# Kernel tuning notes

Measured on AMD Instinct MI355X. Metric: run time of the kernel, lower is better.

Reference implementation:

```python
import jax, jax.numpy as jnp
import numpy as np

B, H, S, D, KG = 1, 8, 1024, 64, 10

def setup_inputs() -> dict:
    key = jax.random.key(0)
    ks = jax.random.split(key, 16)
    n = jax.random.normal
    u = jax.random.uniform
    return {
        'Q': n(ks[0], (B, H, S, D), dtype=jnp.float32),
        'K': n(ks[1], (B, H, S, D), dtype=jnp.float32),
        'V': n(ks[2], (B, H, S, D), dtype=jnp.float32),
        'distance_matrix': u(ks[3], (B, H, S, S), dtype=jnp.float32) * 10.0,
        'energy_matrix': u(ks[4], (B, H, S, S), dtype=jnp.float32) * 5.0,
        'mask': jnp.ones((B, H, S, S), dtype=jnp.int32),
        'mu_D': n(ks[5], (KG,), dtype=jnp.float32),
        'sigma_D': u(ks[6], (KG,), dtype=jnp.float32) + 0.5,  # keep sigma positive
        'b_D': n(ks[7], (KG,), dtype=jnp.float32) * 0.1,
        'mu_E': n(ks[8], (KG,), dtype=jnp.float32),
        'sigma_E': u(ks[9], (KG,), dtype=jnp.float32) + 0.5,
        'b_E': n(ks[10], (KG,), dtype=jnp.float32) * 0.1,
        'W1': n(ks[11], (KG, KG), dtype=jnp.float32) / np.sqrt(KG),
        'b1': jnp.zeros((KG,), dtype=jnp.float32),
        'W2': n(ks[12], (1, KG), dtype=jnp.float32) / np.sqrt(KG),
        'b2': jnp.zeros((1,), dtype=jnp.float32),
    }


def _rbf_mlp_bias(x, b, mu, sigma, W1, b1, W2, b2):
    # x: [B,H,S,S] -> Gaussian RBF features over K kernels, then small MLP -> [B,H,S,S]
    z = (x[..., None] + b - mu) / sigma                      # [B,H,S,S,K]
    inv_norm = 1.0 / (jnp.sqrt(2.0 * jnp.pi) * sigma)
    psi = jnp.exp(-0.5 * z * z) * inv_norm                   # [B,H,S,S,K]
    h = jax.nn.gelu(jnp.einsum('bhijk,lk->bhijl', psi, W1) + b1, approximate=False)
    return (jnp.einsum('bhijk,lk->bhijl', h, W2) + b2)[..., 0]


def reference(Q, K, V, distance_matrix, energy_matrix, mask,
              mu_D, sigma_D, b_D, mu_E, sigma_E, b_E, W1, b1, W2, b2):
    d_model = Q.shape[-1]
    scores = jnp.einsum('bhid,bhjd->bhij', Q, K) / np.sqrt(d_model * 2)
    scores = scores + _rbf_mlp_bias(distance_matrix, b_D, mu_D, sigma_D, W1, b1, W2, b2)
    scores = scores + _rbf_mlp_bias(energy_matrix, b_E, mu_E, sigma_E, W1, b1, W2, b2)
    scores = jnp.where(mask == 0, jnp.float32(-1e9), scores)
    attn = jax.nn.softmax(scores, axis=-1)
    return jnp.einsum('bhij,bhjd->bhid', attn, V)
```

## Files before the change

### kernel.cpp

```cpp
#include <hip/hip_runtime.h>
#include <math.h>

#define Hn 8
#define Sn 1024
#define Dn 64
#define KG 10

#define TN 2048
#define RD 10.25f
#define RE 5.125f

#define KS 4

typedef __attribute__((ext_vector_type(8))) short bf16x8;
typedef __attribute__((ext_vector_type(4))) float f32x4;
typedef unsigned short u16;
typedef unsigned int u32;

__device__ inline float bf2f(u16 u) {
    union { u32 i; float f; } v;
    v.i = ((u32)u) << 16;
    return v.f;
}

__device__ inline u16 f2bf(float f) {
    union { float f; u32 i; } v;
    v.f = f;
    u32 i = v.i;
    return (u16)((i + 0x7FFFu + ((i >> 16) & 1u)) >> 16);
}

__device__ float bias_eval(float x,
                           const float* __restrict__ mu, const float* __restrict__ sg,
                           const float* __restrict__ bb,
                           const float* __restrict__ W1, const float* __restrict__ b1,
                           const float* __restrict__ W2, const float* __restrict__ b2) {
    const float inv_s2pi = 0.39894228040143267794f;
    float psi[KG];
#pragma unroll
    for (int k = 0; k < KG; k++) {
        float s = sg[k];
        float z = (x + bb[k] - mu[k]) / s;
        psi[k] = __expf(-0.5f * z * z) * (inv_s2pi / s);
    }
    float out = b2[0];
#pragma unroll
    for (int l = 0; l < KG; l++) {
        float a = b1[l];
#pragma unroll
        for (int k = 0; k < KG; k++) a += psi[k] * W1[l * KG + k];
        float g = 0.5f * a * (1.0f + erff(a * 0.70710678118654752440f));
        out += g * W2[l];
    }
    return out;
}

#define QK4 262144
#define VTN 524288

__global__ __launch_bounds__(256) void prep_kernel(
    const float* __restrict__ Q, const float* __restrict__ K, const float* __restrict__ V,
    const float* __restrict__ muD, const float* __restrict__ sgD, const float* __restrict__ bD,
    const float* __restrict__ muE, const float* __restrict__ sgE, const float* __restrict__ bE,
    const float* __restrict__ W1, const float* __restrict__ b1,
    const float* __restrict__ W2, const float* __restrict__ b2,
    u32* __restrict__ tab, u16* __restrict__ Qb, u16* __restrict__ Kb, u16* __restrict__ VTi)
{
    int id = blockIdx.x * 256 + threadIdx.x;
    if (id < 2 * TN) {
        int which = (id >= TN);
        int idx = id & (TN - 1);
        float h = (which ? RE : RD) / (float)TN;
        float x0 = idx * h;
        float v0, v1;
        if (which) {
            v0 = bias_eval(x0,     muE, sgE, bE, W1, b1, W2, b2);
            v1 = bias_eval(x0 + h, muE, sgE, bE, W1, b1, W2, b2);
        } else {
            v0 = bias_eval(x0,     muD, sgD, bD, W1, b1, W2, b2);
            v1 = bias_eval(x0 + h, muD, sgD, bD, W1, b1, W2, b2);
        }
        tab[id] = (u32)f2bf(v0) | ((u32)f2bf(v1 - v0) << 16);
    } else if (id < 2 * TN + QK4) {
        int i = id - 2 * TN;
        int arr = i >> 17;
        i &= (1 << 17) - 1;
        float4 v = ((const float4*)(arr ? K : Q))[i];
        ushort4 o;
        o.x = f2bf(v.x); o.y = f2bf(v.y); o.z = f2bf(v.z); o.w = f2bf(v.w);
        ((ushort4*)(arr ? Kb : Qb))[i] = o;
    } else if (id < 2 * TN + QK4 + VTN) {
        int g = id - (2 * TN + QK4);
        int h = g >> 16;
        int d = (g >> 10) & 63;
        int s = g & 1023;
        int t = s >> 5, q = (s >> 3) & 3, j = s & 7;
        int src_s = (t << 5) + (q << 2) + (j & 3) + ((j >> 2) << 4);
        VTi[g] = f2bf(V[(((size_t)h << 10) + src_s) * Dn + d]);
    }
}

__device__ inline float lerp_tab(const u32* __restrict__ st, float x, float invh) {
    float tf = x * invh;
    int i = (int)tf;
    i = max(0, min(i, TN - 1));
    float fr = tf - (float)i;
    u32 p = st[i];
    return fmaf(bf2f((u16)(p >> 16)), fr, bf2f((u16)p));
}

__global__ __launch_bounds__(256, 4) void attn_kernel(
    const u16* __restrict__ Qb, const u16* __restrict__ Kb, const u16* __restrict__ VTi,
    const float* __restrict__ Dm, const float* __restrict__ Em, const int* __restrict__ Mk,
    const u32* __restrict__ gtab,
    float* __restrict__ Up, float* __restrict__ Mp, float* __restrict__ Lp)
{
    __shared__ __align__(16) u32 sTab[2 * TN];
    __shared__ float sO[4][16][68];
    __shared__ float sM[4][16], sL[4][16];

    const int tid = threadIdx.x;
    {
        const uint4* g4 = (const uint4*)gtab;
        uint4* s4 = (uint4*)sTab;
#pragma unroll
        for (int i = 0; i < 4; i++) s4[tid + 256 * i] = g4[tid + 256 * i];
    }
    __syncthreads();

    const int h    = blockIdx.y;
    const int qb   = blockIdx.x;
    const int ks   = blockIdx.z;
    const int q0   = qb * 16;
    const int wave = tid >> 6;
    const int lane = tid & 63;
    const int quad = lane >> 4;
    const int l16  = lane & 15;

    const u16* Qh = Qb  + (size_t)h * Sn * Dn;
    const u16* Kh = Kb  + (size_t)h * Sn * Dn;
    const u16* Vh = VTi + (size_t)h * Dn * Sn;
    const float* Dh = Dm + (size_t)h * Sn * Sn + (size_t)(q0 + l16) * Sn;
    const float* Eh = Em + (size_t)h * Sn * Sn + (size_t)(q0 + l16) * Sn;
    const int*   Mh = Mk + (size_t)h * Sn * Sn + (size_t)(q0 + l16) * Sn;
    const float invhD = (float)TN / RD;
    const float invhE = (float)TN / RE;
    const float scale = 0.08838834764831845f;

    const bf16x8 bQ0 = *(const bf16x8*)(Qh + (q0 + l16) * Dn + quad * 8);
    const bf16x8 bQ1 = *(const bf16x8*)(Qh + (q0 + l16) * Dn + 32 + quad * 8);

    f32x4 O0 = {0.f, 0.f, 0.f, 0.f}, O1 = O0, O2 = O0, O3 = O0;
    float m_run = -1e30f, l_run = 0.f;

    for (int t = 0; t < 2; t++) {
        const int k0 = ks * 256 + wave * 64 + t * 32;

        const float4 Dv0 = *(const float4*)(Dh + k0 + quad * 4);
        const float4 Dv1 = *(const float4*)(Dh + k0 + 16 + quad * 4);
        const float4 Ev0 = *(const float4*)(Eh + k0 + quad * 4);
        const float4 Ev1 = *(const float4*)(Eh + k0 + 16 + quad * 4);
        const int4   Mv0 = *(const int4*)(Mh + k0 + quad * 4);
        const int4   Mv1 = *(const int4*)(Mh + k0 + 16 + quad * 4);

        const u16* kr = Kh + (size_t)(k0 + l16) * Dn + quad * 8;
        const bf16x8 aK00 = *(const bf16x8*)(kr);
        const bf16x8 aK01 = *(const bf16x8*)(kr + 32);
        const bf16x8 aK10 = *(const bf16x8*)(kr + 16 * Dn);
        const bf16x8 aK11 = *(const bf16x8*)(kr + 16 * Dn + 32);

        const u16* vr = Vh + k0 + quad * 8;
        const bf16x8 bV0 = *(const bf16x8*)(vr + (size_t)(l16)      * Sn);
        const bf16x8 bV1 = *(const bf16x8*)(vr + (size_t)(16 + l16) * Sn);
        const bf16x8 bV2 = *(const bf16x8*)(vr + (size_t)(32 + l16) * Sn);
        const bf16x8 bV3 = *(const bf16x8*)(vr + (size_t)(48 + l16) * Sn);

        __builtin_amdgcn_sched_barrier(0);

        f32x4 s0 = {0.f, 0.f, 0.f, 0.f}, s1 = s0;
        s0 = __builtin_amdgcn_mfma_f32_16x16x32_bf16(aK00, bQ0, s0, 0, 0, 0);
        s0 = __builtin_amdgcn_mfma_f32_16x16x32_bf16(aK01, bQ1, s0, 0, 0, 0);
        s1 = __builtin_amdgcn_mfma_f32_16x16x32_bf16(aK10, bQ0, s1, 0, 0, 0);
        s1 = __builtin_amdgcn_mfma_f32_16x16x32_bf16(aK11, bQ1, s1, 0, 0, 0);

        const float dv0[4] = {Dv0.x, Dv0.y, Dv0.z, Dv0.w};
        const float dv1[4] = {Dv1.x, Dv1.y, Dv1.z, Dv1.w};
        const float ev0[4] = {Ev0.x, Ev0.y, Ev0.z, Ev0.w};
        const float ev1[4] = {Ev1.x, Ev1.y, Ev1.z, Ev1.w};
        const int   mv0[4] = {Mv0.x, Mv0.y, Mv0.z, Mv0.w};
        const int   mv1[4] = {Mv1.x, Mv1.y, Mv1.z, Mv1.w};

        float sc0[4], sc1[4];
#pragma unroll
        for (int r = 0; r < 4; r++) {
            float v0 = s0[r] * scale + lerp_tab(sTab, dv0[r], invhD)
                                     + lerp_tab(sTab + TN, ev0[r], invhE);
            v0 = fminf(fmaxf(v0, -80.f), 80.f);
            sc0[r] = (mv0[r] == 0) ? -1e9f : v0;
            float v1 = s1[r] * scale + lerp_tab(sTab, dv1[r], invhD)
                                     + lerp_tab(sTab + TN, ev1[r], invhE);
            v1 = fminf(fmaxf(v1, -80.f), 80.f);
            sc1[r] = (mv1[r] == 0) ? -1e9f : v1;
        }

        float mloc = fmaxf(fmaxf(fmaxf(sc0[0], sc0[1]), fmaxf(sc0[2], sc0[3])),
                           fmaxf(fmaxf(sc1[0], sc1[1]), fmaxf(sc1[2], sc1[3])));
        mloc = fmaxf(mloc, __shfl_xor(mloc, 16, 64));
        mloc = fmaxf(mloc, __shfl_xor(mloc, 32, 64));

        const float mn = fmaxf(m_run, mloc);
        const float al = __expf(m_run - mn);
        m_run = mn;

        float p0[4], p1[4], ll = 0.f;
#pragma unroll
        for (int r = 0; r < 4; r++) {
            p0[r] = __expf(sc0[r] - mn);
            p1[r] = __expf(sc1[r] - mn);
            ll += p0[r] + p1[r];
        }
        ll += __shfl_xor(ll, 16, 64);
        ll += __shfl_xor(ll, 32, 64);
        l_run = l_run * al + ll;

        bf16x8 aP;
#pragma unroll
        for (int r = 0; r < 4; r++) {
            aP[r]     = (short)f2bf(p0[r]);
            aP[4 + r] = (short)f2bf(p1[r]);
        }

        const float a0 = __shfl(al, quad * 4 + 0, 64);
        const float a1 = __shfl(al, quad * 4 + 1, 64);
        const float a2 = __shfl(al, quad * 4 + 2, 64);
        const float a3 = __shfl(al, quad * 4 + 3, 64);
        O0[0] *= a0; O0[1] *= a1; O0[2] *= a2; O0[3] *= a3;
        O1[0] *= a0; O1[1] *= a1; O1[2] *= a2; O1[3] *= a3;
        O2[0] *= a0; O2[1] *= a1; O2[2] *= a2; O2[3] *= a3;
        O3[0] *= a0; O3[1] *= a1; O3[2] *= a2; O3[3] *= a3;

        O0 = __builtin_amdgcn_mfma_f32_16x16x32_bf16(aP, bV0, O0, 0, 0, 0);
        O1 = __builtin_amdgcn_mfma_f32_16x16x32_bf16(aP, bV1, O1, 0, 0, 0);
        O2 = __builtin_amdgcn_mfma_f32_16x16x32_bf16(aP, bV2, O2, 0, 0, 0);
        O3 = __builtin_amdgcn_mfma_f32_16x16x32_bf16(aP, bV3, O3, 0, 0, 0);
    }

    if (lane < 16) {
        sM[wave][lane] = m_run;
        sL[wave][lane] = l_run;
    }
#pragma unroll
    for (int r = 0; r < 4; r++) {
        sO[wave][quad * 4 + r][ 0 + l16] = O0[r];
        sO[wave][quad * 4 + r][16 + l16] = O1[r];
        sO[wave][quad * 4 + r][32 + l16] = O2[r];
        sO[wave][quad * 4 + r][48 + l16] = O3[r];
    }
    __syncthreads();

    const int row = tid >> 4;
    const int c4  = (tid & 15) * 4;
    float mg = sM[0][row];
#pragma unroll
    for (int w = 1; w < 4; w++) mg = fmaxf(mg, sM[w][row]);
    float fac[4], lg = 0.f;
#pragma unroll
    for (int w = 0; w < 4; w++) {
        fac[w] = __expf(sM[w][row] - mg);
        lg += sL[w][row] * fac[w];
    }

    float acc[4];
#pragma unroll
    for (int c = 0; c < 4; c++) {
        acc[c] = 0.f;
#pragma unroll
        for (int w = 0; w < 4; w++) acc[c] += sO[w][row][c4 + c] * fac[w];
    }

    const int pbase = ((h * 64 + qb) * KS + ks) * 16 + row;
    float4 ov = {acc[0], acc[1], acc[2], acc[3]};
    *(float4*)(Up + (size_t)pbase * 64 + c4) = ov;
    if ((tid & 15) == 0) {
        Mp[pbase] = mg;
        Lp[pbase] = lg;
    }
}

__global__ __launch_bounds__(256) void combine_kernel(
    const float* __restrict__ Up, const float* __restrict__ Mp,
    const float* __restrict__ Lp, float* __restrict__ out)
{
    const int g  = blockIdx.x * 256 + threadIdx.x;
    const int r  = g >> 4;
    const int c4 = (g & 15) * 4;
    const int h  = r >> 10;
    const int s  = r & 1023;
    const int qb = s >> 4;
    const int r16 = s & 15;
    const int base = ((h * 64 + qb) * KS) * 16 + r16;

    float m[KS], l[KS];
#pragma unroll
    for (int k = 0; k < KS; k++) {
        m[k] = Mp[base + k * 16];
        l[k] = Lp[base + k * 16];
    }
    float M = m[0];
#pragma unroll
    for (int k = 1; k < KS; k++) M = fmaxf(M, m[k]);
    float f[KS], L = 0.f;
#pragma unroll
    for (int k = 0; k < KS; k++) {
        f[k] = __expf(m[k] - M);
        L += l[k] * f[k];
    }
    const float inv = 1.0f / L;

    float acc[4] = {0.f, 0.f, 0.f, 0.f};
#pragma unroll
    for (int k = 0; k < KS; k++) {
        const float4 u = *(const float4*)(Up + (size_t)(base + k * 16) * 64 + c4);
        acc[0] += u.x * f[k]; acc[1] += u.y * f[k];
        acc[2] += u.z * f[k]; acc[3] += u.w * f[k];
    }
    float4 ov = {acc[0] * inv, acc[1] * inv, acc[2] * inv, acc[3] * inv};
    *(float4*)(out + (size_t)r * Dn + c4) = ov;
}

extern "C" void kernel_launch(void* const* d_in, const int* in_sizes, int n_in,
                              void* d_out, int out_size, void* d_ws, size_t ws_size,
                              hipStream_t stream) {
    const float* Q    = (const float*)d_in[0];
    const float* K    = (const float*)d_in[1];
    const float* V    = (const float*)d_in[2];
    const float* Dm   = (const float*)d_in[3];
    const float* Em   = (const float*)d_in[4];
    const int*   Mask = (const int*)d_in[5];
    const float* muD  = (const float*)d_in[6];
    const float* sgD  = (const float*)d_in[7];
    const float* bD   = (const float*)d_in[8];
    const float* muE  = (const float*)d_in[9];
    const float* sgE  = (const float*)d_in[10];
    const float* bE   = (const float*)d_in[11];
    const float* W1   = (const float*)d_in[12];
    const float* b1   = (const float*)d_in[13];
    const float* W2   = (const float*)d_in[14];
    const float* b2   = (const float*)d_in[15];

    u32* tab = (u32*)d_ws;
    u16* Qb  = (u16*)((char*)d_ws + 2 * TN * 4);
    u16* Kb  = Qb + (size_t)Hn * Sn * Dn;
    u16* VTi = Kb + (size_t)Hn * Sn * Dn;
    float* Up = (float*)(VTi + (size_t)Hn * Sn * Dn);
    float* Mp = Up + (size_t)Hn * 64 * KS * 16 * 64;
    float* Lp = Mp + (size_t)Hn * 64 * KS * 16;

    const int prep_threads = 2 * TN + QK4 + VTN;
    prep_kernel<<<prep_threads / 256, 256, 0, stream>>>(
        Q, K, V, muD, sgD, bD, muE, sgE, bE, W1, b1, W2, b2,
        tab, Qb, Kb, VTi);

    dim3 grid(Sn / 16, Hn, KS);
    attn_kernel<<<grid, 256, 0, stream>>>(Qb, Kb, VTi, Dm, Em, Mask, tab,
                                          Up, Mp, Lp);

    combine_kernel<<<(Hn * Sn * 16) / 256, 256, 0, stream>>>(Up, Mp, Lp,
                                                             (float*)d_out);
}
```

Baseline: 182.1 us.

## Write per-wave partials directly to global and merge all in combine kernel

```diff
diff --git a/kernel.cpp b/kernel.cpp
--- a/kernel.cpp
+++ b/kernel.cpp
@@ -11,6 +11,7 @@
 #define RE 5.125f
 
 #define KS 4
+#define NP (KS * 4)
 
 typedef __attribute__((ext_vector_type(8))) short bf16x8;
 typedef __attribute__((ext_vector_type(4))) float f32x4;
@@ -109,15 +110,13 @@
     return fmaf(bf2f((u16)(p >> 16)), fr, bf2f((u16)p));
 }
 
-__global__ __launch_bounds__(256, 4) void attn_kernel(
+__global__ __launch_bounds__(256, 8) void attn_kernel(
     const u16* __restrict__ Qb, const u16* __restrict__ Kb, const u16* __restrict__ VTi,
     const float* __restrict__ Dm, const float* __restrict__ Em, const int* __restrict__ Mk,
     const u32* __restrict__ gtab,
     float* __restrict__ Up, float* __restrict__ Mp, float* __restrict__ Lp)
 {
     __shared__ __align__(16) u32 sTab[2 * TN];
-    __shared__ float sO[4][16][68];
-    __shared__ float sM[4][16], sL[4][16];
 
     const int tid = threadIdx.x;
     {
@@ -174,8 +173,6 @@
         const bf16x8 bV1 = *(const bf16x8*)(vr + (size_t)(16 + l16) * Sn);
         const bf16x8 bV2 = *(const bf16x8*)(vr + (size_t)(32 + l16) * Sn);
         const bf16x8 bV3 = *(const bf16x8*)(vr + (size_t)(48 + l16) * Sn);
-
-        __builtin_amdgcn_sched_barrier(0);
 
         f32x4 s0 = {0.f, 0.f, 0.f, 0.f}, s1 = s0;
         s0 = __builtin_amdgcn_mfma_f32_16x16x32_bf16(aK00, bQ0, s0, 0, 0, 0);
@@ -245,45 +242,20 @@
         O3 = __builtin_amdgcn_mfma_f32_16x16x32_bf16(aP, bV3, O3, 0, 0, 0);
     }
 
+    const int p = ks * 4 + wave;
+    const size_t pg = (size_t)(h * 64 + qb) * NP + p;
+    float* up = Up + pg * 16 * 64;
+#pragma unroll
+    for (int r = 0; r < 4; r++) {
+        const int row = quad * 4 + r;
+        up[row * 64 +  0 + l16] = O0[r];
+        up[row * 64 + 16 + l16] = O1[r];
+        up[row * 64 + 32 + l16] = O2[r];
+        up[row * 64 + 48 + l16] = O3[r];
+    }
     if (lane < 16) {
-        sM[wave][lane] = m_run;
-        sL[wave][lane] = l_run;
-    }
-#pragma unroll
-    for (int r = 0; r < 4; r++) {
-        sO[wave][quad * 4 + r][ 0 + l16] = O0[r];
-        sO[wave][quad * 4 + r][16 + l16] = O1[r];
-        sO[wave][quad * 4 + r][32 + l16] = O2[r];
-        sO[wave][quad * 4 + r][48 + l16] = O3[r];
-    }
-    __syncthreads();
-
-    const int row = tid >> 4;
-    const int c4  = (tid & 15) * 4;
-    float mg = sM[0][row];
-#pragma unroll
-    for (int w = 1; w < 4; w++) mg = fmaxf(mg, sM[w][row]);
-    float fac[4], lg = 0.f;
-#pragma unroll
-    for (int w = 0; w < 4; w++) {
-        fac[w] = __expf(sM[w][row] - mg);
-        lg += sL[w][row] * fac[w];
-    }
-
-    float acc[4];
-#pragma unroll
-    for (int c = 0; c < 4; c++) {
-        acc[c] = 0.f;
-#pragma unroll
-        for (int w = 0; w < 4; w++) acc[c] += sO[w][row][c4 + c] * fac[w];
-    }
-
-    const int pbase = ((h * 64 + qb) * KS + ks) * 16 + row;
-    float4 ov = {acc[0], acc[1], acc[2], acc[3]};
-    *(float4*)(Up + (size_t)pbase * 64 + c4) = ov;
-    if ((tid & 15) == 0) {
-        Mp[pbase] = mg;
-        Lp[pbase] = lg;
+        Mp[pg * 16 + lane] = m_run;
+        Lp[pg * 16 + lane] = l_run;
     }
 }
 
@@ -298,20 +270,20 @@
     const int s  = r & 1023;
     const int qb = s >> 4;
     const int r16 = s & 15;
-    const int base = ((h * 64 + qb) * KS) * 16 + r16;
-
-    float m[KS], l[KS];
-#pragma unroll
-    for (int k = 0; k < KS; k++) {
-        m[k] = Mp[base + k * 16];
-        l[k] = Lp[base + k * 16];
+    const size_t pg0 = (size_t)(h * 64 + qb) * NP;
+
+    float m[NP], l[NP];
+#pragma unroll
+    for (int k = 0; k < NP; k++) {
+        m[k] = Mp[(pg0 + k) * 16 + r16];
+        l[k] = Lp[(pg0 + k) * 16 + r16];
     }
     float M = m[0];
 #pragma unroll
-    for (int k = 1; k < KS; k++) M = fmaxf(M, m[k]);
-    float f[KS], L = 0.f;
-#pragma unroll
-    for (int k = 0; k < KS; k++) {
+    for (int k = 1; k < NP; k++) M = fmaxf(M, m[k]);
+    float f[NP], L = 0.f;
+#pragma unroll
+    for (int k = 0; k < NP; k++) {
         f[k] = __expf(m[k] - M);
         L += l[k] * f[k];
     }
@@ -319,8 +291,8 @@
 
     float acc[4] = {0.f, 0.f, 0.f, 0.f};
 #pragma unroll
-    for (int k = 0; k < KS; k++) {
-        const float4 u = *(const float4*)(Up + (size_t)(base + k * 16) * 64 + c4);
+    for (int k = 0; k < NP; k++) {
+        const float4 u = *(const float4*)(Up + ((pg0 + k) * 16 + r16) * 64 + c4);
         acc[0] += u.x * f[k]; acc[1] += u.y * f[k];
         acc[2] += u.z * f[k]; acc[3] += u.w * f[k];
     }
@@ -353,8 +325,8 @@
     u16* Kb  = Qb + (size_t)Hn * Sn * Dn;
     u16* VTi = Kb + (size_t)Hn * Sn * Dn;
     float* Up = (float*)(VTi + (size_t)Hn * Sn * Dn);
-    float* Mp = Up + (size_t)Hn * 64 * KS * 16 * 64;
-    float* Lp = Mp + (size_t)Hn * 64 * KS * 16;
+    float* Mp = Up + (size_t)Hn * 64 * NP * 16 * 64;
+    float* Lp = Mp + (size_t)Hn * 64 * NP * 16;
 
     const int prep_threads = 2 * TN + QK4 + VTN;
     prep_kernel<<<prep_threads / 256, 256, 0, stream>>>(
```

Result: slower. 191.0 us (+4.9%).

## Split bias evaluation into separate streaming kernel producing fp16 bias tensor

Applied to the files above, without the earlier changes.

```diff
diff --git a/kernel.cpp b/kernel.cpp
--- a/kernel.cpp
+++ b/kernel.cpp
@@ -14,6 +14,9 @@
 
 typedef __attribute__((ext_vector_type(8))) short bf16x8;
 typedef __attribute__((ext_vector_type(4))) float f32x4;
+typedef _Float16 f16;
+typedef __attribute__((ext_vector_type(4))) _Float16 f16x4;
+typedef __attribute__((ext_vector_type(8))) _Float16 f16x8;
 typedef unsigned short u16;
 typedef unsigned int u32;
 
@@ -109,16 +112,13 @@
     return fmaf(bf2f((u16)(p >> 16)), fr, bf2f((u16)p));
 }
 
-__global__ __launch_bounds__(256, 4) void attn_kernel(
-    const u16* __restrict__ Qb, const u16* __restrict__ Kb, const u16* __restrict__ VTi,
+#define CB_GROUPS (Hn * Sn * Sn / 8)
+
+__global__ __launch_bounds__(256) void bias_kernel(
     const float* __restrict__ Dm, const float* __restrict__ Em, const int* __restrict__ Mk,
-    const u32* __restrict__ gtab,
-    float* __restrict__ Up, float* __restrict__ Mp, float* __restrict__ Lp)
+    const u32* __restrict__ gtab, f16* __restrict__ Cb)
 {
     __shared__ __align__(16) u32 sTab[2 * TN];
-    __shared__ float sO[4][16][68];
-    __shared__ float sM[4][16], sL[4][16];
-
     const int tid = threadIdx.x;
     {
         const uint4* g4 = (const uint4*)gtab;
@@ -127,7 +127,42 @@
         for (int i = 0; i < 4; i++) s4[tid + 256 * i] = g4[tid + 256 * i];
     }
     __syncthreads();
-
+    const float invhD = (float)TN / RD;
+    const float invhE = (float)TN / RE;
+
+    for (int g = blockIdx.x * 256 + tid; g < CB_GROUPS; g += gridDim.x * 256) {
+        const size_t base = (size_t)g * 8;
+
+        const float4 d0 = *(const float4*)(Dm + base);
+        const float4 d1 = *(const float4*)(Dm + base + 4);
+        const float4 e0 = *(const float4*)(Em + base);
+        const float4 e1 = *(const float4*)(Em + base + 4);
+        const int4   m0 = *(const int4*)(Mk + base);
+        const int4   m1 = *(const int4*)(Mk + base + 4);
+
+        const float dv[8] = {d0.x, d0.y, d0.z, d0.w, d1.x, d1.y, d1.z, d1.w};
+        const float ev[8] = {e0.x, e0.y, e0.z, e0.w, e1.x, e1.y, e1.z, e1.w};
+        const int   mv[8] = {m0.x, m0.y, m0.z, m0.w, m1.x, m1.y, m1.z, m1.w};
+
+        f16x8 o;
+#pragma unroll
+        for (int j = 0; j < 8; j++) {
+            float b = lerp_tab(sTab, dv[j], invhD) + lerp_tab(sTab + TN, ev[j], invhE);
+            o[j] = (f16)((mv[j] == 0) ? -60000.0f : b);
+        }
+        ((f16x8*)Cb)[g] = o;
+    }
+}
+
+__global__ __launch_bounds__(256, 6) void attn_kernel(
+    const u16* __restrict__ Qb, const u16* __restrict__ Kb, const u16* __restrict__ VTi,
+    const f16* __restrict__ Cb,
+    float* __restrict__ Up, float* __restrict__ Mp, float* __restrict__ Lp)
+{
+    __shared__ float sO[4][16][68];
+    __shared__ float sM[4][16], sL[4][16];
+
+    const int tid  = threadIdx.x;
     const int h    = blockIdx.y;
     const int qb   = blockIdx.x;
     const int ks   = blockIdx.z;
@@ -140,11 +175,7 @@
     const u16* Qh = Qb  + (size_t)h * Sn * Dn;
     const u16* Kh = Kb  + (size_t)h * Sn * Dn;
     const u16* Vh = VTi + (size_t)h * Dn * Sn;
-    const float* Dh = Dm + (size_t)h * Sn * Sn + (size_t)(q0 + l16) * Sn;
-    const float* Eh = Em + (size_t)h * Sn * Sn + (size_t)(q0 + l16) * Sn;
-    const int*   Mh = Mk + (size_t)h * Sn * Sn + (size_t)(q0 + l16) * Sn;
-    const float invhD = (float)TN / RD;
-    const float invhE = (float)TN / RE;
+    const f16* Ch = Cb  + ((size_t)h * Sn + (q0 + l16)) * Sn;
     const float scale = 0.08838834764831845f;
 
     const bf16x8 bQ0 = *(const bf16x8*)(Qh + (q0 + l16) * Dn + quad * 8);
@@ -156,12 +187,8 @@
     for (int t = 0; t < 2; t++) {
         const int k0 = ks * 256 + wave * 64 + t * 32;
 
-        const float4 Dv0 = *(const float4*)(Dh + k0 + quad * 4);
-        const float4 Dv1 = *(const float4*)(Dh + k0 + 16 + quad * 4);
-        const float4 Ev0 = *(const float4*)(Eh + k0 + quad * 4);
-        const float4 Ev1 = *(const float4*)(Eh + k0 + 16 + quad * 4);
-        const int4   Mv0 = *(const int4*)(Mh + k0 + quad * 4);
-        const int4   Mv1 = *(const int4*)(Mh + k0 + 16 + quad * 4);
+        const f16x4 C0 = *(const f16x4*)(Ch + k0 + quad * 4);
+        const f16x4 C1 = *(const f16x4*)(Ch + k0 + 16 + quad * 4);
 
         const u16* kr = Kh + (size_t)(k0 + l16) * Dn + quad * 8;
         const bf16x8 aK00 = *(const bf16x8*)(kr);
@@ -175,32 +202,17 @@
         const bf16x8 bV2 = *(const bf16x8*)(vr + (size_t)(32 + l16) * Sn);
         const bf16x8 bV3 = *(const bf16x8*)(vr + (size_t)(48 + l16) * Sn);
 
-        __builtin_amdgcn_sched_barrier(0);
-
         f32x4 s0 = {0.f, 0.f, 0.f, 0.f}, s1 = s0;
         s0 = __builtin_amdgcn_mfma_f32_16x16x32_bf16(aK00, bQ0, s0, 0, 0, 0);
         s0 = __builtin_amdgcn_mfma_f32_16x16x32_bf16(aK01, bQ1, s0, 0, 0, 0);
         s1 = __builtin_amdgcn_mfma_f32_16x16x32_bf16(aK10, bQ0, s1, 0, 0, 0);
         s1 = __builtin_amdgcn_mfma_f32_16x16x32_bf16(aK11, bQ1, s1, 0, 0, 0);
 
-        const float dv0[4] = {Dv0.x, Dv0.y, Dv0.z, Dv0.w};
-        const float dv1[4] = {Dv1.x, Dv1.y, Dv1.z, Dv1.w};
-        const float ev0[4] = {Ev0.x, Ev0.y, Ev0.z, Ev0.w};
-        const float ev1[4] = {Ev1.x, Ev1.y, Ev1.z, Ev1.w};
-        const int   mv0[4] = {Mv0.x, Mv0.y, Mv0.z, Mv0.w};
-        const int   mv1[4] = {Mv1.x, Mv1.y, Mv1.z, Mv1.w};
-
         float sc0[4], sc1[4];
 #pragma unroll
         for (int r = 0; r < 4; r++) {
-            float v0 = s0[r] * scale + lerp_tab(sTab, dv0[r], invhD)
-                                     + lerp_tab(sTab + TN, ev0[r], invhE);
-            v0 = fminf(fmaxf(v0, -80.f), 80.f);
-            sc0[r] = (mv0[r] == 0) ? -1e9f : v0;
-            float v1 = s1[r] * scale + lerp_tab(sTab, dv1[r], invhD)
-                                     + lerp_tab(sTab + TN, ev1[r], invhE);
-            v1 = fminf(fmaxf(v1, -80.f), 80.f);
-            sc1[r] = (mv1[r] == 0) ? -1e9f : v1;
+            sc0[r] = fmaf(s0[r], scale, (float)C0[r]);
+            sc1[r] = fmaf(s1[r], scale, (float)C1[r]);
         }
 
         float mloc = fmaxf(fmaxf(fmaxf(sc0[0], sc0[1]), fmaxf(sc0[2], sc0[3])),
@@ -278,12 +290,12 @@
         for (int w = 0; w < 4; w++) acc[c] += sO[w][row][c4 + c] * fac[w];
     }
 
-    const int pbase = ((h * 64 + qb) * KS + ks) * 16 + row;
+    const int pb = (h * 64 + qb) * KS + ks;
     float4 ov = {acc[0], acc[1], acc[2], acc[3]};
-    *(float4*)(Up + (size_t)pbase * 64 + c4) = ov;
+    *(float4*)(Up + (size_t)pb * 1024 + row * 64 + c4) = ov;
     if ((tid & 15) == 0) {
-        Mp[pbase] = mg;
-        Lp[pbase] = lg;
+        Mp[pb * 16 + row] = mg;
+        Lp[pb * 16 + row] = lg;
     }
 }
 
@@ -298,13 +310,13 @@
     const int s  = r & 1023;
     const int qb = s >> 4;
     const int r16 = s & 15;
-    const int base = ((h * 64 + qb) * KS) * 16 + r16;
+    const int pb0 = (h * 64 + qb) * KS;
 
     float m[KS], l[KS];
 #pragma unroll
     for (int k = 0; k < KS; k++) {
-        m[k] = Mp[base + k * 16];
-        l[k] = Lp[base + k * 16];
+        m[k] = Mp[(pb0 + k) * 16 + r16];
+        l[k] = Lp[(pb0 + k) * 16 + r16];
     }
     float M = m[0];
 #pragma unroll
@@ -320,7 +332,7 @@
     float acc[4] = {0.f, 0.f, 0.f, 0.f};
 #pragma unroll
     for (int k = 0; k < KS; k++) {
-        const float4 u = *(const float4*)(Up + (size_t)(base + k * 16) * 64 + c4);
+        const float4 u = *(const float4*)(Up + (size_t)(pb0 + k) * 1024 + r16 * 64 + c4);
         acc[0] += u.x * f[k]; acc[1] += u.y * f[k];
         acc[2] += u.z * f[k]; acc[3] += u.w * f[k];
     }
@@ -352,7 +364,8 @@
     u16* Qb  = (u16*)((char*)d_ws + 2 * TN * 4);
     u16* Kb  = Qb + (size_t)Hn * Sn * Dn;
     u16* VTi = Kb + (size_t)Hn * Sn * Dn;
-    float* Up = (float*)(VTi + (size_t)Hn * Sn * Dn);
+    f16* Cb  = (f16*)(VTi + (size_t)Hn * Sn * Dn);
+    float* Up = (float*)(Cb + (size_t)Hn * Sn * Sn);
     float* Mp = Up + (size_t)Hn * 64 * KS * 16 * 64;
     float* Lp = Mp + (size_t)Hn * 64 * KS * 16;
 
@@ -361,9 +374,10 @@
         Q, K, V, muD, sgD, bD, muE, sgE, bE, W1, b1, W2, b2,
         tab, Qb, Kb, VTi);
 
+    bias_kernel<<<2048, 256, 0, stream>>>(Dm, Em, Mask, tab, Cb);
+
     dim3 grid(Sn / 16, Hn, KS);
-    attn_kernel<<<grid, 256, 0, stream>>>(Qb, Kb, VTi, Dm, Em, Mask, tab,
-                                          Up, Mp, Lp);
+    attn_kernel<<<grid, 256, 0, stream>>>(Qb, Kb, VTi, Cb, Up, Mp, Lp);
 
     combine_kernel<<<(Hn * Sn * 16) / 256, 256, 0, stream>>>(Up, Mp, Lp,
                                                              (float*)d_out);
```

Result: slower. 188.7 us (+3.6%).
